# Kernel tuning notes

Measured on AMD Instinct MI355X. Metric: run time of the kernel, lower is better.

Reference implementation:

```python
import jax, jax.numpy as jnp
import numpy as np

IMG_W = 256
IMG_H = 256
N_PTS = 320
MIN_D = 2.0
MAX_D = 6.0
FOCAL = 2.0          # f = 1/tan(fov/2), fov ~ 53 deg
EPS_EA = 1e-10       # pytorch3d EmissionAbsorption eps
EPS = 1e-8           # module's normalization eps
DENSITY = 0.1        # constant density used when opacity is None


def trilinear_sample(vol, pts):
    """grid_sample-style trilinear, align_corners=True, zero padding.
    vol: (D,H,W); pts: (...,3) local coords (x->W, y->H, z->D) in [-1,1]."""
    D, H, W = vol.shape
    x, y, z = pts[..., 0], pts[..., 1], pts[..., 2]
    ix = (x + 1.0) * 0.5 * (W - 1)
    iy = (y + 1.0) * 0.5 * (H - 1)
    iz = (z + 1.0) * 0.5 * (D - 1)
    x0f, y0f, z0f = jnp.floor(ix), jnp.floor(iy), jnp.floor(iz)
    fx, fy, fz = ix - x0f, iy - y0f, iz - z0f
    x0 = x0f.astype(jnp.int32); x1 = x0 + 1
    y0 = y0f.astype(jnp.int32); y1 = y0 + 1
    z0 = z0f.astype(jnp.int32); z1 = z0 + 1
    out = jnp.zeros_like(ix)
    for zi, wz in ((z0, 1.0 - fz), (z1, fz)):
        for yi, wy in ((y0, 1.0 - fy), (y1, fy)):
            for xi, wx in ((x0, 1.0 - fx), (x1, fx)):
                valid = (xi >= 0) & (xi < W) & (yi >= 0) & (yi < H) & (zi >= 0) & (zi < D)
                v = vol[jnp.clip(zi, 0, D - 1), jnp.clip(yi, 0, H - 1), jnp.clip(xi, 0, W - 1)]
                out = out + jnp.where(valid, v * (wz * wy * wx), 0.0)
    return out


def setup_inputs() -> dict:
    key = jax.random.key(0)
    image3d = jax.random.uniform(key, (1, 1, 256, 256, 256), dtype=jnp.float32)
    R = jnp.eye(3, dtype=jnp.float32)[None]                 # (1,3,3) extrinsic rotation
    T = jnp.array([[0.0, 0.0, 4.0]], dtype=jnp.float32)     # (1,3) camera at z=-4 world
    return {"image3d": image3d, "R": R, "T": T}


def reference(image3d, R, T):
    B, C, D, H, W = image3d.shape
    vol = image3d[:, 0]                                     # (B,D,H,W); RGB repeat -> channels equal
    shape = max(C, D)
    vox = 3.0 / shape
    # --- NDC ray sampling (uniform depths) ---
    yg, xg = jnp.meshgrid(jnp.linspace(-1.0, 1.0, IMG_H),
                          jnp.linspace(-1.0, 1.0, IMG_W), indexing='ij')   # (IH,IW)
    depths = jnp.linspace(MIN_D, MAX_D, N_PTS)
    xcam = xg[..., None] * depths / FOCAL                   # (IH,IW,P)
    ycam = yg[..., None] * depths / FOCAL
    zcam = jnp.broadcast_to(depths, xcam.shape)
    pcam = jnp.stack([xcam, ycam, zcam], axis=-1)           # (IH,IW,P,3)
    # world points: X_cam = X_world @ R + T  =>  X_world = (X_cam - T) @ R^T
    v = pcam[None] - T[:, None, None, None, :]              # (B,IH,IW,P,3)
    pw = jnp.einsum('bhwpj,bkj->bhwpk', v, R)
    # world -> volume local coords (align_corners=True span over voxel centers)
    half = jnp.array([vox * (W - 1) * 0.5, vox * (H - 1) * 0.5, vox * (D - 1) * 0.5], jnp.float32)
    local = pw / half                                       # (B,IH,IW,P,3)
    # --- trilinear gather of features & densities ---
    feat = jax.vmap(trilinear_sample)(vol, local)           # (B,IH,IW,P)
    ones_vol = jnp.ones((D, H, W), jnp.float32)
    sigma = DENSITY * jax.vmap(trilinear_sample, in_axes=(None, 0))(ones_vol, local)
    # --- emission-absorption front-to-back compositing ---
    t = (1.0 + EPS_EA) - sigma
    absorption = jnp.cumprod(t, axis=-1)
    absorption = jnp.concatenate([jnp.ones_like(absorption[..., :1]), absorption[..., :-1]], axis=-1)
    weights = sigma * absorption
    rgb = jnp.sum(weights * feat, axis=-1)                  # (B,IH,IW); RGB channels identical
    # permute(0,3,2,1) then mean over 3 identical RGB channels -> (B,1,IW,IH)
    out = jnp.transpose(rgb, (0, 2, 1))[:, None]
    # norm_type == 'standardized': normalized(standardized(x))
    s = (out - out.mean()) / (jnp.std(out, ddof=1) + EPS)
    out = (s - s.min() + EPS) / (s.max() - s.min() + EPS)
    return out
```

## Files before the change

kernel.cpp:

```cpp
#include <hip/hip_runtime.h>

#define NPTS 320
#define NCHUNK 8
#define CHUNK (NPTS / NCHUNK)
#define PIX_PER_BLOCK 64
#define D0 2.0f
#define DSTEP (4.0f / 319.0f)
#define HALFV (765.0f / 512.0f)
#define DENSITY_C 0.1f

__global__ __launch_bounds__(512, 6)
void render_kernel(const float* __restrict__ vol,
                   const float* __restrict__ R,
                   const float* __restrict__ T,
                   float* __restrict__ raw,
                   float* __restrict__ bsum,
                   float* __restrict__ bsumsq,
                   float* __restrict__ bmin,
                   float* __restrict__ bmax) {
  const int lane  = threadIdx.x & 63;
  const int chunk = threadIdx.x >> 6;
  const int pixel = blockIdx.x * PIX_PER_BLOCK + lane;
  const int h = pixel >> 8;
  const int w = pixel & 255;

  const float xh = (w * (2.0f / 255.0f) - 1.0f) * 0.5f;
  const float yh = (h * (2.0f / 255.0f) - 1.0f) * 0.5f;

  const float R00 = R[0], R01 = R[1], R02 = R[2];
  const float R10 = R[3], R11 = R[4], R12 = R[5];
  const float R20 = R[6], R21 = R[7], R22 = R[8];
  const float T0 = T[0], T1 = T[1], T2 = T[2];

  const float S = 127.5f / HALFV;
  const float Cx = R00 * xh + R01 * yh + R02;
  const float Cy = R10 * xh + R11 * yh + R12;
  const float Cz = R20 * xh + R21 * yh + R22;
  const float Kx = -(R00 * T0 + R01 * T1 + R02 * T2);
  const float Ky = -(R10 * T0 + R11 * T1 + R12 * T2);
  const float Kz = -(R20 * T0 + R21 * T1 + R22 * T2);
  const float ax = Cx * S, bx = Kx * S + 127.5f;
  const float ay = Cy * S, by = Ky * S + 127.5f;
  const float az = Cz * S, bz = Kz * S + 127.5f;
  const float ix0 = ax * D0 + bx, dix = ax * DSTEP;
  const float iy0 = ay * D0 + by, diy = ay * DSTEP;
  const float iz0 = az * D0 + bz, diz = az * DSTEP;

  float plo_in = -1e9f, phi_in = 1e9f, plo_out = -1e9f, phi_out = 1e9f;
  auto slab = [](float a, float b, float L, float H, float& lo, float& hi) {
    if (fabsf(a) < 1e-5f) {
      if (b < L || b > H) { lo = 1e9f; hi = -1e9f; }
    } else {
      const float p1 = (L - b) / a, p2 = (H - b) / a;
      lo = fmaxf(lo, fminf(p1, p2));
      hi = fminf(hi, fmaxf(p1, p2));
    }
  };
  slab(dix, ix0, 0.01f, 254.99f, plo_in, phi_in);
  slab(diy, iy0, 0.01f, 254.99f, plo_in, phi_in);
  slab(diz, iz0, 0.01f, 254.99f, plo_in, phi_in);
  slab(dix, ix0, -1.01f, 256.01f, plo_out, phi_out);
  slab(diy, iy0, -1.01f, 256.01f, plo_out, phi_out);
  slab(diz, iz0, -1.01f, 256.01f, plo_out, phi_out);

  const int i_in_lo  = (int)ceilf(fminf(fmaxf(plo_in, 0.0f), 320.0f));
  const int i_in_hi  = (int)floorf(fminf(fmaxf(phi_in, -1.0f), 319.0f)) + 1;
  const int i_out_lo = (int)ceilf(fminf(fmaxf(plo_out, 0.0f), 320.0f));
  const int i_out_hi = (int)floorf(fminf(fmaxf(phi_out, -1.0f), 319.0f)) + 1;

  float acc = 0.0f;
  float Tac = 1.0f;
  const int p0 = chunk * CHUNK;

  auto masked_sample = [&](int p) {
    const float pf = (float)p;
    const float ix = fmaf(pf, dix, ix0);
    const float iy = fmaf(pf, diy, iy0);
    const float iz = fmaf(pf, diz, iz0);
    if (ix > -1.0f && ix < 256.0f && iy > -1.0f && iy < 256.0f &&
        iz > -1.0f && iz < 256.0f) {
      const float xf = floorf(ix), yf = floorf(iy), zf = floorf(iz);
      const float fx = ix - xf, fy = iy - yf, fz = iz - zf;
      const int x0 = (int)xf, y0 = (int)yf, z0 = (int)zf;
      const float wx0 = (x0 >= 0)   ? 1.0f - fx : 0.0f;
      const float wx1 = (x0 <= 254) ? fx        : 0.0f;
      const float wy0 = (y0 >= 0)   ? 1.0f - fy : 0.0f;
      const float wy1 = (y0 <= 254) ? fy        : 0.0f;
      const float wz0 = (z0 >= 0)   ? 1.0f - fz : 0.0f;
      const float wz1 = (z0 <= 254) ? fz        : 0.0f;
      const int xc0 = max(x0, 0),     xc1 = min(x0 + 1, 255);
      const int yc0 = max(y0, 0),     yc1 = min(y0 + 1, 255);
      const int zc0 = max(z0, 0),     zc1 = min(z0 + 1, 255);
      const int b00 = (zc0 * 256 + yc0) * 256;
      const int b01 = (zc0 * 256 + yc1) * 256;
      const int b10 = (zc1 * 256 + yc0) * 256;
      const int b11 = (zc1 * 256 + yc1) * 256;
      const float v000 = vol[b00 + xc0], v001 = vol[b00 + xc1];
      const float v010 = vol[b01 + xc0], v011 = vol[b01 + xc1];
      const float v100 = vol[b10 + xc0], v101 = vol[b10 + xc1];
      const float v110 = vol[b11 + xc0], v111 = vol[b11 + xc1];
      const float fs =
          wz0 * (wy0 * (wx0 * v000 + wx1 * v001) +
                 wy1 * (wx0 * v010 + wx1 * v011)) +
          wz1 * (wy0 * (wx0 * v100 + wx1 * v101) +
                 wy1 * (wx0 * v110 + wx1 * v111));
      const float wsum  = (wx0 + wx1) * (wy0 + wy1) * (wz0 + wz1);
      const float sigma = DENSITY_C * wsum;
      acc = fmaf(sigma * Tac, fs, acc);
      Tac *= (1.0f + 1e-10f - sigma);
    } else {
      Tac *= (1.0f + 1e-10f);
    }
  };

  auto fast_sample = [&](int p) -> float {
    const float pf = (float)p;
    const float ix = fmaf(pf, dix, ix0);
    const float iy = fmaf(pf, diy, iy0);
    const float iz = fmaf(pf, diz, iz0);
    const int x0 = (int)ix, y0 = (int)iy, z0 = (int)iz;
    const float fx = ix - (float)x0;
    const float fy = iy - (float)y0;
    const float fz = iz - (float)z0;
    const int base = (z0 << 16) + (y0 << 8) + x0;
    const float v000 = vol[base],         v001 = vol[base + 1];
    const float v010 = vol[base + 256],   v011 = vol[base + 257];
    const float v100 = vol[base + 65536], v101 = vol[base + 65537];
    const float v110 = vol[base + 65792], v111 = vol[base + 65793];
    const float c00 = fmaf(fx, v001 - v000, v000);
    const float c01 = fmaf(fx, v011 - v010, v010);
    const float c10 = fmaf(fx, v101 - v100, v100);
    const float c11 = fmaf(fx, v111 - v110, v110);
    const float c0  = fmaf(fy, c01 - c00, c00);
    const float c1  = fmaf(fy, c11 - c10, c10);
    return fmaf(fz, c1 - c0, c0);
  };

  const int lo_o = max(p0, i_out_lo);
  const int hi_o = min(p0 + CHUNK, i_out_hi);
  const int lo_f = min(max(lo_o, i_in_lo), hi_o);
  const int hi_f = min(max(lo_f, i_in_hi), hi_o);

  for (int p = lo_o; p < lo_f; ++p) masked_sample(p);

  int p = lo_f;
#pragma unroll 1
  for (; p + 4 <= hi_f; p += 4) {
    const float fs0 = fast_sample(p);
    const float fs1 = fast_sample(p + 1);
    const float fs2 = fast_sample(p + 2);
    const float fs3 = fast_sample(p + 3);
    const float g = fmaf(0.729f, fs3,
                    fmaf(0.81f,  fs2,
                    fmaf(0.9f,   fs1, fs0)));
    acc = fmaf(Tac * DENSITY_C, g, acc);
    Tac *= 0.6561f;
  }
  for (; p < hi_f; ++p) {
    const float fs = fast_sample(p);
    acc = fmaf(Tac * DENSITY_C, fs, acc);
    Tac *= (1.0f - DENSITY_C);
  }

  for (p = hi_f; p < hi_o; ++p) masked_sample(p);

  __shared__ float lrgb[NCHUNK][PIX_PER_BLOCK];
  __shared__ float lT[NCHUNK][PIX_PER_BLOCK];
  lrgb[chunk][lane] = acc;
  lT[chunk][lane]   = Tac;
  __syncthreads();

  if (threadIdx.x < 64) {
    float a = 0.0f, Tp = 1.0f;
#pragma unroll
    for (int c = 0; c < NCHUNK; ++c) {
      a  = fmaf(Tp, lrgb[c][lane], a);
      Tp *= lT[c][lane];
    }
    raw[pixel] = a;

    float s = a, q = a * a, mn = a, mx = a;
#pragma unroll
    for (int off = 32; off > 0; off >>= 1) {
      s += __shfl_down(s, off, 64);
      q += __shfl_down(q, off, 64);
      mn = fminf(mn, __shfl_down(mn, off, 64));
      mx = fmaxf(mx, __shfl_down(mx, off, 64));
    }
    if (lane == 0) {
      bsum[blockIdx.x]   = s;
      bsumsq[blockIdx.x] = q;
      bmin[blockIdx.x]   = mn;
      bmax[blockIdx.x]   = mx;
    }
  }
}

__global__ __launch_bounds__(1024)
void finalize_kernel(const float* __restrict__ raw,
                     const float* __restrict__ bsum,
                     const float* __restrict__ bsumsq,
                     const float* __restrict__ bmin,
                     const float* __restrict__ bmax,
                     float* __restrict__ out) {
  __shared__ double sS[1024];
  __shared__ double sQ[1024];
  __shared__ float sMn[1024], sMx[1024];
  const int t = threadIdx.x;
  sS[t] = (double)bsum[t];
  sQ[t] = (double)bsumsq[t];
  sMn[t] = bmin[t];
  sMx[t] = bmax[t];
  __syncthreads();
  for (int off = 512; off > 0; off >>= 1) {
    if (t < off) {
      sS[t] += sS[t + off];
      sQ[t] += sQ[t + off];
      sMn[t] = fminf(sMn[t], sMn[t + off]);
      sMx[t] = fmaxf(sMx[t], sMx[t + off]);
    }
    __syncthreads();
  }
  const double N = 65536.0;
  const double sum = sS[0], sumsq = sQ[0];
  const double mean = sum / N;
  double var = (sumsq - sum * sum / N) / (N - 1.0);
  if (var < 0.0) var = 0.0;
  const float stdeps = (float)sqrt(var) + 1e-8f;
  const float inv_std = 1.0f / stdeps;
  const float fmean = (float)mean;
  const float smin = (sMn[0] - fmean) * inv_std;
  const float smax = (sMx[0] - fmean) * inv_std;
  const float inv_range = 1.0f / (smax - smin + 1e-8f);

  const int o = blockIdx.x * 1024 + t;
  const int wq = o >> 8;
  const int hq = o & 255;
  const float s = (raw[hq * 256 + wq] - fmean) * inv_std;
  out[o] = (s - smin + 1e-8f) * inv_range;
}

extern "C" void kernel_launch(void* const* d_in, const int* in_sizes, int n_in,
                              void* d_out, int out_size, void* d_ws, size_t ws_size,
                              hipStream_t stream) {
  const float* vol = (const float*)d_in[0];
  const float* R   = (const float*)d_in[1];
  const float* T   = (const float*)d_in[2];
  float* out = (float*)d_out;

  float* raw    = (float*)d_ws;
  float* bsum   = raw + 65536;
  float* bsumsq = bsum + 1024;
  float* bmin   = bsumsq + 1024;
  float* bmax   = bmin + 1024;

  render_kernel<<<1024, 512, 0, stream>>>(vol, R, T, raw, bsum, bsumsq, bmin, bmax);
  finalize_kernel<<<64, 1024, 0, stream>>>(raw, bsum, bsumsq, bmin, bmax, out);
}
```

Before: 120.8 us.

## Balance ray chunks over valid range, pair voxel loads, shuffle-based finalize

Each ray's 8 wave chunks now split only the valid sample range [i_out_lo, i_out_hi) instead of fixed 40-point slices, so no wave sits idle on samples outside the volume. Trilinear corner fetches are merged into four 2-float vector loads with 4-byte alignment. Launch bounds rise to 8 waves per SIMD. The finalize kernel swaps the shared-memory tree over 1024 entries for wave shuffles across 256-thread blocks. Risks include register pressure from the higher occupancy target, and the chunk ordering in the compositing combine must still match the new boundaries.

```diff
diff --git a/kernel.cpp b/kernel.cpp
--- a/kernel.cpp
+++ b/kernel.cpp
@@ -2,14 +2,15 @@
 
 #define NPTS 320
 #define NCHUNK 8
-#define CHUNK (NPTS / NCHUNK)
 #define PIX_PER_BLOCK 64
 #define D0 2.0f
 #define DSTEP (4.0f / 319.0f)
 #define HALFV (765.0f / 512.0f)
 #define DENSITY_C 0.1f
 
-__global__ __launch_bounds__(512, 6)
+typedef float f2a __attribute__((ext_vector_type(2), aligned(4)));
+
+__global__ __launch_bounds__(512, 8)
 void render_kernel(const float* __restrict__ vol,
                    const float* __restrict__ R,
                    const float* __restrict__ T,
@@ -68,9 +69,13 @@
   const int i_out_lo = (int)ceilf(fminf(fmaxf(plo_out, 0.0f), 320.0f));
   const int i_out_hi = (int)floorf(fminf(fmaxf(phi_out, -1.0f), 319.0f)) + 1;
 
+  const int rlo = max(0, i_out_lo);
+  const int L   = max(0, min(NPTS, i_out_hi) - rlo);
+  const int lo_o = rlo + ((chunk * L) >> 3);
+  const int hi_o = rlo + (((chunk + 1) * L) >> 3);
+
   float acc = 0.0f;
   float Tac = 1.0f;
-  const int p0 = chunk * CHUNK;
 
   auto masked_sample = [&](int p) {
     const float pf = (float)p;
@@ -123,21 +128,19 @@
     const float fy = iy - (float)y0;
     const float fz = iz - (float)z0;
     const int base = (z0 << 16) + (y0 << 8) + x0;
-    const float v000 = vol[base],         v001 = vol[base + 1];
-    const float v010 = vol[base + 256],   v011 = vol[base + 257];
-    const float v100 = vol[base + 65536], v101 = vol[base + 65537];
-    const float v110 = vol[base + 65792], v111 = vol[base + 65793];
-    const float c00 = fmaf(fx, v001 - v000, v000);
-    const float c01 = fmaf(fx, v011 - v010, v010);
-    const float c10 = fmaf(fx, v101 - v100, v100);
-    const float c11 = fmaf(fx, v111 - v110, v110);
+    const f2a v00 = *(const f2a*)(vol + base);
+    const f2a v01 = *(const f2a*)(vol + base + 256);
+    const f2a v10 = *(const f2a*)(vol + base + 65536);
+    const f2a v11 = *(const f2a*)(vol + base + 65792);
+    const float c00 = fmaf(fx, v00.y - v00.x, v00.x);
+    const float c01 = fmaf(fx, v01.y - v01.x, v01.x);
+    const float c10 = fmaf(fx, v10.y - v10.x, v10.x);
+    const float c11 = fmaf(fx, v11.y - v11.x, v11.x);
     const float c0  = fmaf(fy, c01 - c00, c00);
     const float c1  = fmaf(fy, c11 - c10, c10);
     return fmaf(fz, c1 - c0, c0);
   };
 
-  const int lo_o = max(p0, i_out_lo);
-  const int hi_o = min(p0 + CHUNK, i_out_hi);
   const int lo_f = min(max(lo_o, i_in_lo), hi_o);
   const int hi_f = min(max(lo_f, i_in_hi), hi_o);
 
@@ -196,48 +199,58 @@
   }
 }
 
-__global__ __launch_bounds__(1024)
+__global__ __launch_bounds__(256)
 void finalize_kernel(const float* __restrict__ raw,
                      const float* __restrict__ bsum,
                      const float* __restrict__ bsumsq,
                      const float* __restrict__ bmin,
                      const float* __restrict__ bmax,
                      float* __restrict__ out) {
-  __shared__ double sS[1024];
-  __shared__ double sQ[1024];
-  __shared__ float sMn[1024], sMx[1024];
+  __shared__ double wS[4], wQ[4];
+  __shared__ float wMn[4], wMx[4];
   const int t = threadIdx.x;
-  sS[t] = (double)bsum[t];
-  sQ[t] = (double)bsumsq[t];
-  sMn[t] = bmin[t];
-  sMx[t] = bmax[t];
+  const int lane = t & 63, wv = t >> 6;
+
+  double s = 0.0, q = 0.0;
+  float mn = 3.4e38f, mx = -3.4e38f;
+#pragma unroll
+  for (int i = 0; i < 4; ++i) {
+    const int idx = t + i * 256;
+    s += (double)bsum[idx];
+    q += (double)bsumsq[idx];
+    mn = fminf(mn, bmin[idx]);
+    mx = fmaxf(mx, bmax[idx]);
+  }
+#pragma unroll
+  for (int off = 32; off > 0; off >>= 1) {
+    s += __shfl_down(s, off, 64);
+    q += __shfl_down(q, off, 64);
+    mn = fminf(mn, __shfl_down(mn, off, 64));
+    mx = fmaxf(mx, __shfl_down(mx, off, 64));
+  }
+  if (lane == 0) { wS[wv] = s; wQ[wv] = q; wMn[wv] = mn; wMx[wv] = mx; }
   __syncthreads();
-  for (int off = 512; off > 0; off >>= 1) {
-    if (t < off) {
-      sS[t] += sS[t + off];
-      sQ[t] += sQ[t + off];
-      sMn[t] = fminf(sMn[t], sMn[t + off]);
-      sMx[t] = fmaxf(sMx[t], sMx[t + off]);
-    }
-    __syncthreads();
-  }
+  const double sum   = wS[0] + wS[1] + wS[2] + wS[3];
+  const double sumsq = wQ[0] + wQ[1] + wQ[2] + wQ[3];
+  const float  gmn = fminf(fminf(wMn[0], wMn[1]), fminf(wMn[2], wMn[3]));
+  const float  gmx = fmaxf(fmaxf(wMx[0], wMx[1]), fmaxf(wMx[2], wMx[3]));
+
   const double N = 65536.0;
-  const double sum = sS[0], sumsq = sQ[0];
   const double mean = sum / N;
   double var = (sumsq - sum * sum / N) / (N - 1.0);
   if (var < 0.0) var = 0.0;
   const float stdeps = (float)sqrt(var) + 1e-8f;
   const float inv_std = 1.0f / stdeps;
   const float fmean = (float)mean;
-  const float smin = (sMn[0] - fmean) * inv_std;
-  const float smax = (sMx[0] - fmean) * inv_std;
+  const float smin = (gmn - fmean) * inv_std;
+  const float smax = (gmx - fmean) * inv_std;
   const float inv_range = 1.0f / (smax - smin + 1e-8f);
 
-  const int o = blockIdx.x * 1024 + t;
+  const int o = blockIdx.x * 256 + t;
   const int wq = o >> 8;
   const int hq = o & 255;
-  const float s = (raw[hq * 256 + wq] - fmean) * inv_std;
-  out[o] = (s - smin + 1e-8f) * inv_range;
+  const float sv = (raw[hq * 256 + wq] - fmean) * inv_std;
+  out[o] = (sv - smin + 1e-8f) * inv_range;
 }
 
 extern "C" void kernel_launch(void* const* d_in, const int* in_sizes, int n_in,
@@ -255,5 +268,5 @@
   float* bmax   = bmin + 1024;
 
   render_kernel<<<1024, 512, 0, stream>>>(vol, R, T, raw, bsum, bsumsq, bmin, bmax);
-  finalize_kernel<<<64, 1024, 0, stream>>>(raw, bsum, bsumsq, bmin, bmax, out);
+  finalize_kernel<<<256, 256, 0, stream>>>(raw, bsum, bsumsq, bmin, bmax, out);
 }
```

New measurement: 171.3 us. 1.42x slower.
